# Optimization experiments

Hardware: AMD Instinct MI355X
Metric: run time of the kernel (lower is better)

The kernel has to match this reference:

```python
import jax, jax.numpy as jnp
import numpy as np

B, S_ENC, S_DEC, ENC_H, DEC_H = 8, 2048, 2048, 512, 512


def setup_inputs() -> dict:
    key = jax.random.key(0)
    k1, k2, k3 = jax.random.split(key, 3)
    return {
        "enc_hidden_states": jax.random.normal(k1, (B, S_ENC, ENC_H), dtype=jnp.float32),
        "dec_hidden_states": jax.random.normal(k2, (B, S_DEC, DEC_H), dtype=jnp.float32),
        "W_att": jax.random.normal(k3, (ENC_H, DEC_H), dtype=jnp.float32),
    }


def reference(enc_hidden_states, dec_hidden_states, W_att):
    # Project encoder states: [B, S_enc, dec_h]
    enc_proj = jnp.einsum("bse,ed->bsd", enc_hidden_states, W_att)
    # Luong 'general' scores for all decoder timesteps at once: [B, S_dec, S_enc]
    # (original code loops over decoder timesteps via tf.map_fn; this is the
    # equivalent single batched matmul)
    att_logits = jnp.einsum("btd,bsd->bts", dec_hidden_states, enc_proj)
    att_softmax = jax.nn.softmax(att_logits, axis=-1)
    # Attention context vectors: [B, S_dec, enc_h]
    att_vector = jnp.einsum("bts,bse->bte", att_softmax, enc_hidden_states)
    return att_vector
```

## Files before the change

kernel.cpp:

```cpp
#include <hip/hip_runtime.h>
#include <cstdint>


#define DEVINL __device__ __forceinline__

typedef __attribute__((ext_vector_type(8))) short short8;
typedef __attribute__((ext_vector_type(4))) float f32x4;

DEVINL short f2bf(float x) {
    union { float f; uint32_t u; } v; v.f = x;
    uint32_t r = v.u + 0x7FFFu + ((v.u >> 16) & 1u);
    return (short)(r >> 16);
}
DEVINL float bf2f(short h) {
    union { uint32_t u; float f; } v; v.u = ((uint32_t)(uint16_t)h) << 16;
    return v.f;
}

DEVINL void gload_lds16(const void* g, void* l) {
    __builtin_amdgcn_global_load_lds(
        (const __attribute__((address_space(1))) char*)g,
        (__attribute__((address_space(3))) char*)l, 16, 0, 0);
}

__global__ __launch_bounds__(256)
void split_kernel(const float* __restrict__ x, short* __restrict__ hi,
                  short* __restrict__ lo)
{
    long i = ((long)blockIdx.x * 256 + threadIdx.x) * 8;
    f32x4 a = *(const f32x4*)(x + i);
    f32x4 b = *(const f32x4*)(x + i + 4);
    short8 h, l;
#pragma unroll
    for (int j = 0; j < 4; j++) {
        short ha = f2bf(a[j]); h[j] = ha;     l[j] = f2bf(a[j] - bf2f(ha));
        short hb = f2bf(b[j]); h[4 + j] = hb; l[4 + j] = f2bf(b[j] - bf2f(hb));
    }
    *(short8*)(hi + i) = h;
    *(short8*)(lo + i) = l;
}

__global__ __launch_bounds__(256)
void split_w_kernel(const float* __restrict__ w, short* __restrict__ wth,
                    short* __restrict__ wtl)
{
    int idx = blockIdx.x * 256 + threadIdx.x;
    int k = idx >> 9, n = idx & 511;
    float v = w[idx];
    short h = f2bf(v);
    wth[(long)n * 512 + k] = h;
    wtl[(long)n * 512 + k] = f2bf(v - bf2f(h));
}

__global__ __launch_bounds__(256)
void split_transpose_kernel(const float* __restrict__ x, short* __restrict__ hi,
                            short* __restrict__ lo, short* __restrict__ xt)
{
    __shared__ short tile[32][33];
    const int b  = blockIdx.z;
    const int s0 = blockIdx.x * 32;
    const int e0 = blockIdx.y * 32;
    const float* px = x + (long)b * 2048 * 512;
    short* ph = hi + (long)b * 2048 * 512;
    short* pl = lo + (long)b * 2048 * 512;
    short* pt = xt + (long)b * 512 * 2048;
    const int tx = threadIdx.x & 31;
    const int ty = threadIdx.x >> 5;
#pragma unroll
    for (int r = 0; r < 32; r += 8) {
        long idx = (long)(s0 + ty + r) * 512 + e0 + tx;
        float v = px[idx];
        short h = f2bf(v);
        ph[idx] = h;
        pl[idx] = f2bf(v - bf2f(h));
        tile[ty + r][tx] = h;
    }
    __syncthreads();
#pragma unroll
    for (int r = 0; r < 32; r += 8)
        pt[(long)(e0 + ty + r) * 2048 + s0 + tx] = tile[tx][ty + r];
}

template<int NTERMS, bool SPLIT_OUT>
__global__ __launch_bounds__(256, 2)
void gemm_bt(const short* __restrict__ Ah, const short* __restrict__ Al,
             const short* __restrict__ Bh, const short* __restrict__ Bl,
             float* __restrict__ C, short* __restrict__ Ch, short* __restrict__ Cl,
             int K, int lda, int ldb, int ldc,
             long sA, long sB, long sC)
{
    extern __shared__ char smem_raw[];
    constexpr int OPS = (NTERMS == 3) ? 4 : 2;
    constexpr int SET = 128 * 32 * OPS;
    short* smem = (short*)smem_raw;

    const int tid  = threadIdx.x;
    const int wave = tid >> 6;
    const int lane = tid & 63;
    const int quad = lane >> 4;
    const int l16  = lane & 15;
    const int wm   = (wave >> 1) * 64;
    const int wn   = (wave & 1) * 64;

    const long tile_m = (long)blockIdx.y * 128;
    const long tile_n = (long)blockIdx.x * 128;
    const int  bz     = blockIdx.z;

    const short* pAh = Ah + (long)bz * sA;
    const short* pBh = Bh + (long)bz * sB;
    const short* pAl = (NTERMS == 3) ? (Al + (long)bz * sA) : nullptr;
    const short* pBl = (NTERMS == 3) ? (Bl + (long)bz * sB) : nullptr;

    const int srow = tid >> 2;
    const int skq  = (tid & 3) * 8;
    const int lds_off = srow * 32 + skq;
    const long ga0 = (tile_m + srow) * (long)lda + skq;
    const long gb0 = (tile_n + srow) * (long)ldb + skq;

    auto stage = [&](int k0, int buf) {
        short* s   = smem + buf * SET;
        short* ash = s;
        short* bsh = s + 128 * 32;
        gload_lds16(pAh + ga0 + k0,             ash + lds_off);
        gload_lds16(pAh + ga0 + 64l * lda + k0, ash + lds_off + 64 * 32);
        gload_lds16(pBh + gb0 + k0,             bsh + lds_off);
        gload_lds16(pBh + gb0 + 64l * ldb + k0, bsh + lds_off + 64 * 32);
        if constexpr (NTERMS == 3) {
            short* asl = s + 2 * 128 * 32;
            short* bsl = s + 3 * 128 * 32;
            gload_lds16(pAl + ga0 + k0,             asl + lds_off);
            gload_lds16(pAl + ga0 + 64l * lda + k0, asl + lds_off + 64 * 32);
            gload_lds16(pBl + gb0 + k0,             bsl + lds_off);
            gload_lds16(pBl + gb0 + 64l * ldb + k0, bsl + lds_off + 64 * 32);
        }
    };

    f32x4 acc[4][4] = {};
    stage(0, 0);
    int cur = 0;

    for (int k0 = 0; k0 < K; k0 += 32) {
        __syncthreads();
        if (k0 + 32 < K) stage(k0 + 32, cur ^ 1);

        short* s   = smem + cur * SET;
        short* ash = s;
        short* bsh = s + 128 * 32;
        short* asl = s + 2 * 128 * 32;
        short* bsl = s + 3 * 128 * 32;

        short8 ah[4], bh[4], al[4], bl[4];
#pragma unroll
        for (int i = 0; i < 4; i++) {
            ah[i] = *(const short8*)&ash[(wm + i * 16 + l16) * 32 + quad * 8];
            bh[i] = *(const short8*)&bsh[(wn + i * 16 + l16) * 32 + quad * 8];
            if constexpr (NTERMS == 3) {
                al[i] = *(const short8*)&asl[(wm + i * 16 + l16) * 32 + quad * 8];
                bl[i] = *(const short8*)&bsl[(wn + i * 16 + l16) * 32 + quad * 8];
            }
        }
#pragma unroll
        for (int i = 0; i < 4; i++)
#pragma unroll
            for (int j = 0; j < 4; j++) {
                acc[i][j] = __builtin_amdgcn_mfma_f32_16x16x32_bf16(ah[i], bh[j], acc[i][j], 0, 0, 0);
                if constexpr (NTERMS == 3) {
                    acc[i][j] = __builtin_amdgcn_mfma_f32_16x16x32_bf16(ah[i], bl[j], acc[i][j], 0, 0, 0);
                    acc[i][j] = __builtin_amdgcn_mfma_f32_16x16x32_bf16(al[i], bh[j], acc[i][j], 0, 0, 0);
                }
            }
        cur ^= 1;
    }

#pragma unroll
    for (int i = 0; i < 4; i++)
#pragma unroll
        for (int j = 0; j < 4; j++) {
            const long row0 = tile_m + wm + i * 16 + quad * 4;
            const long col  = tile_n + wn + j * 16 + l16;
#pragma unroll
            for (int r = 0; r < 4; r++) {
                float v = acc[i][j][r];
                if constexpr (SPLIT_OUT) {
                    long idx = (long)bz * sC + (row0 + r) * (long)ldc + col;
                    short h = f2bf(v);
                    Ch[idx] = h;
                    Cl[idx] = f2bf(v - bf2f(h));
                } else {
                    C[(long)bz * sC + (row0 + r) * (long)ldc + col] = v;
                }
            }
        }
}

__global__ __launch_bounds__(512, 2)
void gemm3_256(const short* __restrict__ Ah, const short* __restrict__ Al,
               const short* __restrict__ Bh, const short* __restrict__ Bl,
               short* __restrict__ Pt, float* __restrict__ stats,
               int K, int lda, int ldb,
               long sA, long sB, int nbx, int nby)
{
    extern __shared__ char smem_raw[];
    short* smem = (short*)smem_raw;
    constexpr int PL  = 256 * 32;
    constexpr int SET = 4 * PL;

    const int t    = threadIdx.x;
    const int wave = t >> 6;
    const int lane = t & 63;
    const int quad = lane >> 4;
    const int l16  = lane & 15;
    const int wm   = (wave >> 2) * 128;
    const int wn   = (wave & 3) * 64;
    const int kslot8 = ((quad ^ ((l16 >> 1) & 3)) << 3);

    const int nwg = gridDim.x;
    const int wg  = blockIdx.x;
    const int swz = (wg & 7) * (nwg >> 3) + (wg >> 3);
    const int per_b = nbx * nby;
    const int bz  = swz / per_b;
    const int rem = swz - bz * per_b;
    const long tile_m = (long)(rem / nbx) * 256;
    const long tile_n = (long)(rem % nbx) * 256;

    const short* pAh = Ah + (long)bz * sA;
    const short* pAl = Al + (long)bz * sA;
    const short* pBh = Bh + (long)bz * sB;
    const short* pBl = Bl + (long)bz * sB;

    const int srow   = t >> 2;
    const int schunk = (t & 3) ^ ((t >> 3) & 3);
    const long gA  = (tile_m + srow) * (long)lda + schunk * 8;
    const long gB  = (tile_n + srow) * (long)ldb + schunk * 8;
    const long gA2 = gA + 128l * lda;
    const long gB2 = gB + 128l * ldb;
    const int ld0 = t * 8;

    f32x4 acc[8][4] = {};

    {
        short* s = smem;
        gload_lds16(pAh + gA,  s + ld0);
        gload_lds16(pAh + gA2, s + ld0 + 4096);
        gload_lds16(pBh + gB,  s + 2 * PL + ld0);
        gload_lds16(pBh + gB2, s + 2 * PL + ld0 + 4096);
        gload_lds16(pAl + gA,  s + PL + ld0);
        gload_lds16(pAl + gA2, s + PL + ld0 + 4096);
        gload_lds16(pBl + gB,  s + 3 * PL + ld0);
        gload_lds16(pBl + gB2, s + 3 * PL + ld0 + 4096);
    }
    asm volatile("s_waitcnt vmcnt(4)" ::: "memory");
    __builtin_amdgcn_s_barrier();

    const int NT = K >> 5;
    int cur = 0;
#pragma unroll 1
    for (int kt = 0; kt < NT; ++kt) {
        const short* s    = smem + cur * SET;
        short* sn         = smem + (cur ^ 1) * SET;
        const short* ah_p = s;
        const short* al_p = s + PL;
        const short* bh_p = s + 2 * PL;
        const short* bl_p = s + 3 * PL;
        const int  k0n  = (kt + 1) << 5;
        const bool more = (kt + 1 < NT);

        short8 ahA[4], ahB[4], xbh[4], xbl[4], xal[4];

#pragma unroll
        for (int i = 0; i < 4; i++)
            ahA[i] = *(const short8*)&ah_p[(wm + i * 16 + l16) * 32 + kslot8];
#pragma unroll
        for (int j = 0; j < 4; j++)
            xbh[j] = *(const short8*)&bh_p[(wn + j * 16 + l16) * 32 + kslot8];
        if (more) {
            gload_lds16(pAh + gA  + k0n, sn + ld0);
            gload_lds16(pAh + gA2 + k0n, sn + ld0 + 4096);
        }
        __builtin_amdgcn_s_barrier();
        asm volatile("s_waitcnt lgkmcnt(0)" ::: "memory");
        __builtin_amdgcn_sched_barrier(0);
        __builtin_amdgcn_s_setprio(1);
#pragma unroll
        for (int i = 0; i < 4; i++)
#pragma unroll
            for (int j = 0; j < 4; j++)
                acc[i][j] = __builtin_amdgcn_mfma_f32_16x16x32_bf16(ahA[i], xbh[j], acc[i][j], 0, 0, 0);
        __builtin_amdgcn_s_setprio(0);

#pragma unroll
        for (int i = 0; i < 4; i++)
            ahB[i] = *(const short8*)&ah_p[(wm + 64 + i * 16 + l16) * 32 + kslot8];
        if (more) {
            gload_lds16(pBh + gB  + k0n, sn + 2 * PL + ld0);
            gload_lds16(pBh + gB2 + k0n, sn + 2 * PL + ld0 + 4096);
            asm volatile("s_waitcnt vmcnt(6)" ::: "memory");
        } else {
            asm volatile("s_waitcnt vmcnt(2)" ::: "memory");
        }
        __builtin_amdgcn_s_barrier();
        asm volatile("s_waitcnt lgkmcnt(0)" ::: "memory");
        __builtin_amdgcn_sched_barrier(0);
        __builtin_amdgcn_s_setprio(1);
#pragma unroll
        for (int i = 0; i < 4; i++)
#pragma unroll
            for (int j = 0; j < 4; j++)
                acc[4 + i][j] = __builtin_amdgcn_mfma_f32_16x16x32_bf16(ahB[i], xbh[j], acc[4 + i][j], 0, 0, 0);
        __builtin_amdgcn_s_setprio(0);

#pragma unroll
        for (int i = 0; i < 4; i++)
            xal[i] = *(const short8*)&al_p[(wm + i * 16 + l16) * 32 + kslot8];
        if (more) {
            gload_lds16(pAl + gA  + k0n, sn + PL + ld0);
            gload_lds16(pAl + gA2 + k0n, sn + PL + ld0 + 4096);
        }
        __builtin_amdgcn_s_barrier();
        asm volatile("s_waitcnt lgkmcnt(0)" ::: "memory");
        __builtin_amdgcn_sched_barrier(0);
        __builtin_amdgcn_s_setprio(1);
#pragma unroll
        for (int i = 0; i < 4; i++)
#pragma unroll
            for (int j = 0; j < 4; j++)
                acc[i][j] = __builtin_amdgcn_mfma_f32_16x16x32_bf16(xal[i], xbh[j], acc[i][j], 0, 0, 0);
        __builtin_amdgcn_s_setprio(0);

#pragma unroll
        for (int i = 0; i < 4; i++)
            xal[i] = *(const short8*)&al_p[(wm + 64 + i * 16 + l16) * 32 + kslot8];
        if (more) {
            gload_lds16(pBl + gB  + k0n, sn + 3 * PL + ld0);
            gload_lds16(pBl + gB2 + k0n, sn + 3 * PL + ld0 + 4096);
            asm volatile("s_waitcnt vmcnt(8)" ::: "memory");
        } else {
            asm volatile("s_waitcnt vmcnt(0)" ::: "memory");
        }
        __builtin_amdgcn_s_barrier();
        asm volatile("s_waitcnt lgkmcnt(0)" ::: "memory");
        __builtin_amdgcn_sched_barrier(0);
        __builtin_amdgcn_s_setprio(1);
#pragma unroll
        for (int i = 0; i < 4; i++)
#pragma unroll
            for (int j = 0; j < 4; j++)
                acc[4 + i][j] = __builtin_amdgcn_mfma_f32_16x16x32_bf16(xal[i], xbh[j], acc[4 + i][j], 0, 0, 0);
        __builtin_amdgcn_s_setprio(0);

#pragma unroll
        for (int j = 0; j < 4; j++)
            xbl[j] = *(const short8*)&bl_p[(wn + j * 16 + l16) * 32 + kslot8];
        __builtin_amdgcn_s_barrier();
        asm volatile("s_waitcnt lgkmcnt(0)" ::: "memory");
        __builtin_amdgcn_sched_barrier(0);
        __builtin_amdgcn_s_setprio(1);
#pragma unroll
        for (int i = 0; i < 4; i++)
#pragma unroll
            for (int j = 0; j < 4; j++)
                acc[i][j] = __builtin_amdgcn_mfma_f32_16x16x32_bf16(ahA[i], xbl[j], acc[i][j], 0, 0, 0);
        __builtin_amdgcn_s_setprio(0);

        __builtin_amdgcn_s_setprio(1);
#pragma unroll
        for (int i = 0; i < 4; i++)
#pragma unroll
            for (int j = 0; j < 4; j++)
                acc[4 + i][j] = __builtin_amdgcn_mfma_f32_16x16x32_bf16(ahB[i], xbl[j], acc[4 + i][j], 0, 0, 0);
        __builtin_amdgcn_s_setprio(0);
        if (more) {
            asm volatile("s_waitcnt vmcnt(4)" ::: "memory");
            __builtin_amdgcn_s_barrier();
        }

        cur ^= 1;
    }

    float* sf   = (float*)smem_raw;
    float* lmax = sf;
    float* rowm = sf + 1024;
    const int wr = wave >> 2, wc = wave & 3;
    __syncthreads();

#pragma unroll
    for (int i = 0; i < 8; i++)
#pragma unroll
        for (int r = 0; r < 4; r++) {
            float m = acc[i][0][r];
#pragma unroll
            for (int j = 1; j < 4; j++) m = fmaxf(m, acc[i][j][r]);
#pragma unroll
            for (int o = 1; o < 16; o <<= 1) m = fmaxf(m, __shfl_xor(m, o));
            if (l16 == 0) lmax[wc * 256 + wr * 128 + i * 16 + quad * 4 + r] = m;
        }
    __syncthreads();
    if (t < 256)
        rowm[t] = fmaxf(fmaxf(lmax[t], lmax[256 + t]),
                        fmaxf(lmax[512 + t], lmax[768 + t]));
    __syncthreads();
    float* lsum = sf;
    short* PtB  = Pt + (long)bz * 2048 * 2048;
#pragma unroll
    for (int i = 0; i < 8; i++)
#pragma unroll
        for (int r = 0; r < 4; r++) {
            const int rit = wr * 128 + i * 16 + quad * 4 + r;
            const float m = rowm[rit];
            float sum = 0.f;
#pragma unroll
            for (int j = 0; j < 4; j++) {
                float e = __expf(acc[i][j][r] - m);
                sum += e;
                PtB[(tile_m + rit) * 2048 + tile_n + wn + j * 16 + l16] = f2bf(e);
            }
#pragma unroll
            for (int o = 1; o < 16; o <<= 1) sum += __shfl_xor(sum, o);
            if (l16 == 0) lsum[wc * 256 + rit] = sum;
        }
    __syncthreads();
    if (t < 256) {
        float S = lsum[t] + lsum[256 + t] + lsum[512 + t] + lsum[768 + t];
        const long sidx = (((long)bz * 2048 + tile_m + t) * 8 + (tile_n >> 8)) * 2;
        stats[sidx]     = rowm[t];
        stats[sidx + 1] = S;
    }
}

__global__ __launch_bounds__(256)
void combine_kernel(const float* __restrict__ stats, float* __restrict__ scales)
{
    const long row = (long)blockIdx.x * 256 + threadIdx.x;
    const float* p = stats + row * 16;
    float m[8], s[8];
#pragma unroll
    for (int t = 0; t < 8; t++) { m[t] = p[t * 2]; s[t] = p[t * 2 + 1]; }
    float M = m[0];
#pragma unroll
    for (int t = 1; t < 8; t++) M = fmaxf(M, m[t]);
    float S = 0.f;
#pragma unroll
    for (int t = 0; t < 8; t++) S += s[t] * __expf(m[t] - M);
    const float inv = 1.f / S;
#pragma unroll
    for (int t = 0; t < 8; t++)
        scales[row * 8 + t] = __expf(m[t] - M) * inv;
}

__global__ __launch_bounds__(256, 2)
void gemm_pv(const short* __restrict__ A, const short* __restrict__ B,
             const float* __restrict__ scales, float* __restrict__ C,
             int K, int lda, int ldb, int ldc,
             long sA, long sB, long sC)
{
    extern __shared__ char smem_raw[];
    constexpr int SET = 128 * 32 * 2;
    short* smem = (short*)smem_raw;

    const int tid  = threadIdx.x;
    const int wave = tid >> 6;
    const int lane = tid & 63;
    const int quad = lane >> 4;
    const int l16  = lane & 15;
    const int wm   = (wave >> 1) * 64;
    const int wn   = (wave & 1) * 64;

    const long tile_m = (long)blockIdx.y * 128;
    const long tile_n = (long)blockIdx.x * 128;
    const int  bz     = blockIdx.z;

    const short* pA = A + (long)bz * sA;
    const short* pB = B + (long)bz * sB;

    const int srow = tid >> 2;
    const int skq  = (tid & 3) * 8;
    const int lds_off = srow * 32 + skq;
    const long ga0 = (tile_m + srow) * (long)lda + skq;
    const long gb0 = (tile_n + srow) * (long)ldb + skq;

    auto stage = [&](int k0, int buf) {
        short* s   = smem + buf * SET;
        short* ash = s;
        short* bsh = s + 128 * 32;
        gload_lds16(pA + ga0 + k0,             ash + lds_off);
        gload_lds16(pA + ga0 + 64l * lda + k0, ash + lds_off + 64 * 32);
        gload_lds16(pB + gb0 + k0,             bsh + lds_off);
        gload_lds16(pB + gb0 + 64l * ldb + k0, bsh + lds_off + 64 * 32);
    };

    f32x4 acc[4][4] = {};
    f32x4 oacc[4][4] = {};
    const f32x4 vzero = {0.f, 0.f, 0.f, 0.f};
    stage(0, 0);
    int cur = 0;

    for (int k0 = 0; k0 < K; k0 += 32) {
        __syncthreads();
        if (k0 + 32 < K) stage(k0 + 32, cur ^ 1);

        short* s   = smem + cur * SET;
        short* ash = s;
        short* bsh = s + 128 * 32;

        short8 ah[4], bh[4];
#pragma unroll
        for (int i = 0; i < 4; i++) {
            ah[i] = *(const short8*)&ash[(wm + i * 16 + l16) * 32 + quad * 8];
            bh[i] = *(const short8*)&bsh[(wn + i * 16 + l16) * 32 + quad * 8];
        }
#pragma unroll
        for (int i = 0; i < 4; i++)
#pragma unroll
            for (int j = 0; j < 4; j++)
                acc[i][j] = __builtin_amdgcn_mfma_f32_16x16x32_bf16(ah[i], bh[j], acc[i][j], 0, 0, 0);

        if (((k0 + 32) & 255) == 0) {
            const int tt = k0 >> 8;
#pragma unroll
            for (int i = 0; i < 4; i++) {
                f32x4 sv;
#pragma unroll
                for (int r = 0; r < 4; r++)
                    sv[r] = scales[((long)bz * 2048 + tile_m + wm + i * 16 + quad * 4 + r) * 8 + tt];
#pragma unroll
                for (int j = 0; j < 4; j++) {
                    oacc[i][j] += sv * acc[i][j];
                    acc[i][j] = vzero;
                }
            }
        }
        cur ^= 1;
    }

#pragma unroll
    for (int i = 0; i < 4; i++)
#pragma unroll
        for (int j = 0; j < 4; j++) {
            const long row0 = tile_m + wm + i * 16 + quad * 4;
            const long col  = tile_n + wn + j * 16 + l16;
#pragma unroll
            for (int r = 0; r < 4; r++)
                C[(long)bz * sC + (row0 + r) * (long)ldc + col] = oacc[i][j][r];
        }
}

extern "C" void kernel_launch(void* const* d_in, const int* in_sizes, int n_in,
                              void* d_out, int out_size, void* d_ws, size_t ws_size,
                              hipStream_t stream)
{
    const float* enc = (const float*)d_in[0];
    const float* dec = (const float*)d_in[1];
    const float* W   = (const float*)d_in[2];
    float* out = (float*)d_out;

    const long BSE = 8l * 2048 * 512;
    const long NW  = 512l * 512;

    char* p = (char*)d_ws;
    auto take = [&](long bytes) { char* r = p; p += (bytes + 255) & ~255l; return r; };
    short* enc_hi = (short*)take(BSE * 2);
    short* enc_lo = (short*)take(BSE * 2);
    short* dec_hi = (short*)take(BSE * 2);
    short* dec_lo = (short*)take(BSE * 2);
    short* ep_hi  = (short*)take(BSE * 2);
    short* ep_lo  = (short*)take(BSE * 2);
    short* enc_t  = (short*)take(BSE * 2);
    short* wt_hi  = (short*)take(NW * 2);
    short* wt_lo  = (short*)take(NW * 2);
    short* Pt     = (short*)take(8l * 2048 * 2048 * 2);
    float* stats  = (float*)take(8l * 2048 * 8 * 2 * 4);
    float* scales = (float*)take(8l * 2048 * 8 * 4);
    (void)ws_size; (void)in_sizes; (void)n_in; (void)out_size;

    static bool attr_set = false;
    if (!attr_set) {
        (void)hipFuncSetAttribute((const void*)gemm3_256,
                                  hipFuncAttributeMaxDynamicSharedMemorySize,
                                  131072);
        attr_set = true;
    }

    split_transpose_kernel<<<dim3(64, 16, 8), 256, 0, stream>>>(
        enc, enc_hi, enc_lo, enc_t);
    split_kernel<<<4096, 256, 0, stream>>>(dec, dec_hi, dec_lo);
    split_w_kernel<<<1024, 256, 0, stream>>>(W, wt_hi, wt_lo);

    gemm_bt<3, true><<<dim3(4, 128, 1), 256, 64 * 1024, stream>>>(
        enc_hi, enc_lo, wt_hi, wt_lo, nullptr, ep_hi, ep_lo,
        512, 512, 512, 512, 0, 0, 0);

    gemm3_256<<<512, 512, 131072, stream>>>(
        dec_hi, dec_lo, ep_hi, ep_lo, Pt, stats,
        512, 512, 512, 2048l * 512, 2048l * 512, 8, 8);

    combine_kernel<<<64, 256, 0, stream>>>(stats, scales);

    gemm_pv<<<dim3(4, 16, 8), 256, 32 * 1024, stream>>>(
        Pt, enc_t, scales, out,
        2048, 2048, 2048, 512, 2048l * 2048, 512l * 2048, 2048l * 512);
}
```

Measured before the change: 319.5 us.

## Fuse decoder fp32-to-bf16 hi/lo split into the score GEMM A-tile loader

Drops the separate split kernel for decoder states. The score GEMM now reads fp32 decoder rows directly into registers, splits them into bf16 hi/lo inside the kernel and writes both to LDS. This removes one launch and a full round trip of bf16 hi/lo decoder data through global memory. In exchange the GEMM reads twice the A bytes as fp32, spends extra VALU on the conversion, and reorders its vmcnt waits in the pipeline, which adds register pressure and latency risk.

```diff
diff --git a/kernel.cpp b/kernel.cpp
--- a/kernel.cpp
+++ b/kernel.cpp
@@ -21,23 +21,6 @@
     __builtin_amdgcn_global_load_lds(
         (const __attribute__((address_space(1))) char*)g,
         (__attribute__((address_space(3))) char*)l, 16, 0, 0);
-}
-
-__global__ __launch_bounds__(256)
-void split_kernel(const float* __restrict__ x, short* __restrict__ hi,
-                  short* __restrict__ lo)
-{
-    long i = ((long)blockIdx.x * 256 + threadIdx.x) * 8;
-    f32x4 a = *(const f32x4*)(x + i);
-    f32x4 b = *(const f32x4*)(x + i + 4);
-    short8 h, l;
-#pragma unroll
-    for (int j = 0; j < 4; j++) {
-        short ha = f2bf(a[j]); h[j] = ha;     l[j] = f2bf(a[j] - bf2f(ha));
-        short hb = f2bf(b[j]); h[4 + j] = hb; l[4 + j] = f2bf(b[j] - bf2f(hb));
-    }
-    *(short8*)(hi + i) = h;
-    *(short8*)(lo + i) = l;
 }
 
 __global__ __launch_bounds__(256)
@@ -194,11 +177,9 @@
 }
 
 __global__ __launch_bounds__(512, 2)
-void gemm3_256(const short* __restrict__ Ah, const short* __restrict__ Al,
-               const short* __restrict__ Bh, const short* __restrict__ Bl,
-               short* __restrict__ Pt, float* __restrict__ stats,
-               int K, int lda, int ldb,
-               long sA, long sB, int nbx, int nby)
+void gemm3_256(const float* __restrict__ Dec, const short* __restrict__ Bh,
+               const short* __restrict__ Bl, short* __restrict__ Pt,
+               float* __restrict__ stats, int nbx, int nby)
 {
     extern __shared__ char smem_raw[];
     short* smem = (short*)smem_raw;
@@ -223,39 +204,68 @@
     const long tile_m = (long)(rem / nbx) * 256;
     const long tile_n = (long)(rem % nbx) * 256;
 
-    const short* pAh = Ah + (long)bz * sA;
-    const short* pAl = Al + (long)bz * sA;
-    const short* pBh = Bh + (long)bz * sB;
-    const short* pBl = Bl + (long)bz * sB;
+    const float* pDec = Dec + (long)bz * 2048 * 512;
+    const short* pBh  = Bh + (long)bz * 2048 * 512;
+    const short* pBl  = Bl + (long)bz * 2048 * 512;
 
     const int srow   = t >> 2;
     const int schunk = (t & 3) ^ ((t >> 3) & 3);
-    const long gA  = (tile_m + srow) * (long)lda + schunk * 8;
-    const long gB  = (tile_n + srow) * (long)ldb + schunk * 8;
-    const long gA2 = gA + 128l * lda;
-    const long gB2 = gB + 128l * ldb;
+    const long gB  = (tile_n + srow) * 512l + schunk * 8;
+    const long gB2 = gB + 128l * 512;
     const int ld0 = t * 8;
 
+    const int srowA = t >> 1;
+    const int kA0   = (t & 1) * 16;
+    const long gAf  = (tile_m + srowA) * 512l + kA0;
+    const int xrA   = (srowA >> 1) & 3;
+    const int c0    = kA0 >> 3;
+    const int wA0   = srowA * 32 + ((c0 ^ xrA) << 3);
+    const int wA1   = srowA * 32 + (((c0 + 1) ^ xrA) << 3);
+
+    f32x4 af[4];
+    auto loadA = [&](int k0) {
+#pragma unroll
+        for (int q = 0; q < 4; q++)
+            af[q] = *(const f32x4*)(pDec + gAf + k0 + q * 4);
+    };
+    auto writeA = [&](int buf) {
+        short8 h0, h1, l0, l1;
+#pragma unroll
+        for (int e = 0; e < 8; e++) {
+            float v = af[e >> 2][e & 3];
+            short hh = f2bf(v);
+            h0[e] = hh; l0[e] = f2bf(v - bf2f(hh));
+        }
+#pragma unroll
+        for (int e = 0; e < 8; e++) {
+            float v = af[2 + (e >> 2)][e & 3];
+            short hh = f2bf(v);
+            h1[e] = hh; l1[e] = f2bf(v - bf2f(hh));
+        }
+        short* sp = smem + buf * SET;
+        *(short8*)&sp[wA0]      = h0;
+        *(short8*)&sp[wA1]      = h1;
+        *(short8*)&sp[PL + wA0] = l0;
+        *(short8*)&sp[PL + wA1] = l1;
+    };
+
     f32x4 acc[8][4] = {};
 
-    {
-        short* s = smem;
-        gload_lds16(pAh + gA,  s + ld0);
-        gload_lds16(pAh + gA2, s + ld0 + 4096);
-        gload_lds16(pBh + gB,  s + 2 * PL + ld0);
-        gload_lds16(pBh + gB2, s + 2 * PL + ld0 + 4096);
-        gload_lds16(pAl + gA,  s + PL + ld0);
-        gload_lds16(pAl + gA2, s + PL + ld0 + 4096);
-        gload_lds16(pBl + gB,  s + 3 * PL + ld0);
-        gload_lds16(pBl + gB2, s + 3 * PL + ld0 + 4096);
-    }
-    asm volatile("s_waitcnt vmcnt(4)" ::: "memory");
+    loadA(0);
+    __builtin_amdgcn_sched_barrier(0);
+    gload_lds16(pBh + gB,  smem + 2 * PL + ld0);
+    gload_lds16(pBh + gB2, smem + 2 * PL + ld0 + 4096);
+    gload_lds16(pBl + gB,  smem + 3 * PL + ld0);
+    gload_lds16(pBl + gB2, smem + 3 * PL + ld0 + 4096);
+    __builtin_amdgcn_sched_barrier(0);
+    asm volatile("s_waitcnt vmcnt(2)" ::: "memory");
+    writeA(0);
+    asm volatile("s_waitcnt lgkmcnt(0)" ::: "memory");
     __builtin_amdgcn_s_barrier();
 
-    const int NT = K >> 5;
     int cur = 0;
 #pragma unroll 1
-    for (int kt = 0; kt < NT; ++kt) {
+    for (int kt = 0; kt < 16; ++kt) {
         const short* s    = smem + cur * SET;
         short* sn         = smem + (cur ^ 1) * SET;
         const short* ah_p = s;
@@ -263,7 +273,7 @@
         const short* bh_p = s + 2 * PL;
         const short* bl_p = s + 3 * PL;
         const int  k0n  = (kt + 1) << 5;
-        const bool more = (kt + 1 < NT);
+        const bool more = (kt + 1 < 16);
 
         short8 ahA[4], ahB[4], xbh[4], xbl[4], xal[4];
 
@@ -273,10 +283,6 @@
 #pragma unroll
         for (int j = 0; j < 4; j++)
             xbh[j] = *(const short8*)&bh_p[(wn + j * 16 + l16) * 32 + kslot8];
-        if (more) {
-            gload_lds16(pAh + gA  + k0n, sn + ld0);
-            gload_lds16(pAh + gA2 + k0n, sn + ld0 + 4096);
-        }
         __builtin_amdgcn_s_barrier();
         asm volatile("s_waitcnt lgkmcnt(0)" ::: "memory");
         __builtin_amdgcn_sched_barrier(0);
@@ -294,9 +300,6 @@
         if (more) {
             gload_lds16(pBh + gB  + k0n, sn + 2 * PL + ld0);
             gload_lds16(pBh + gB2 + k0n, sn + 2 * PL + ld0 + 4096);
-            asm volatile("s_waitcnt vmcnt(6)" ::: "memory");
-        } else {
-            asm volatile("s_waitcnt vmcnt(2)" ::: "memory");
         }
         __builtin_amdgcn_s_barrier();
         asm volatile("s_waitcnt lgkmcnt(0)" ::: "memory");
@@ -313,8 +316,10 @@
         for (int i = 0; i < 4; i++)
             xal[i] = *(const short8*)&al_p[(wm + i * 16 + l16) * 32 + kslot8];
         if (more) {
-            gload_lds16(pAl + gA  + k0n, sn + PL + ld0);
-            gload_lds16(pAl + gA2 + k0n, sn + PL + ld0 + 4096);
+            loadA(k0n);
+            __builtin_amdgcn_sched_barrier(0);
+            gload_lds16(pBl + gB  + k0n, sn + 3 * PL + ld0);
+            gload_lds16(pBl + gB2 + k0n, sn + 3 * PL + ld0 + 4096);
         }
         __builtin_amdgcn_s_barrier();
         asm volatile("s_waitcnt lgkmcnt(0)" ::: "memory");
@@ -330,13 +335,10 @@
 #pragma unroll
         for (int i = 0; i < 4; i++)
             xal[i] = *(const short8*)&al_p[(wm + 64 + i * 16 + l16) * 32 + kslot8];
-        if (more) {
-            gload_lds16(pBl + gB  + k0n, sn + 3 * PL + ld0);
-            gload_lds16(pBl + gB2 + k0n, sn + 3 * PL + ld0 + 4096);
+        if (more)
             asm volatile("s_waitcnt vmcnt(8)" ::: "memory");
-        } else {
+        else
             asm volatile("s_waitcnt vmcnt(0)" ::: "memory");
-        }
         __builtin_amdgcn_s_barrier();
         asm volatile("s_waitcnt lgkmcnt(0)" ::: "memory");
         __builtin_amdgcn_sched_barrier(0);
@@ -351,6 +353,10 @@
 #pragma unroll
         for (int j = 0; j < 4; j++)
             xbl[j] = *(const short8*)&bl_p[(wn + j * 16 + l16) * 32 + kslot8];
+        if (more) {
+            asm volatile("s_waitcnt vmcnt(2)" ::: "memory");
+            writeA(cur ^ 1);
+        }
         __builtin_amdgcn_s_barrier();
         asm volatile("s_waitcnt lgkmcnt(0)" ::: "memory");
         __builtin_amdgcn_sched_barrier(0);
@@ -369,10 +375,8 @@
             for (int j = 0; j < 4; j++)
                 acc[4 + i][j] = __builtin_amdgcn_mfma_f32_16x16x32_bf16(ahB[i], xbl[j], acc[4 + i][j], 0, 0, 0);
         __builtin_amdgcn_s_setprio(0);
-        if (more) {
-            asm volatile("s_waitcnt vmcnt(4)" ::: "memory");
+        if (more)
             __builtin_amdgcn_s_barrier();
-        }
 
         cur ^= 1;
     }
@@ -560,8 +564,6 @@
     auto take = [&](long bytes) { char* r = p; p += (bytes + 255) & ~255l; return r; };
     short* enc_hi = (short*)take(BSE * 2);
     short* enc_lo = (short*)take(BSE * 2);
-    short* dec_hi = (short*)take(BSE * 2);
-    short* dec_lo = (short*)take(BSE * 2);
     short* ep_hi  = (short*)take(BSE * 2);
     short* ep_lo  = (short*)take(BSE * 2);
     short* enc_t  = (short*)take(BSE * 2);
@@ -582,7 +584,6 @@
 
     split_transpose_kernel<<<dim3(64, 16, 8), 256, 0, stream>>>(
         enc, enc_hi, enc_lo, enc_t);
-    split_kernel<<<4096, 256, 0, stream>>>(dec, dec_hi, dec_lo);
     split_w_kernel<<<1024, 256, 0, stream>>>(W, wt_hi, wt_lo);
 
     gemm_bt<3, true><<<dim3(4, 128, 1), 256, 64 * 1024, stream>>>(
@@ -590,8 +591,7 @@
         512, 512, 512, 512, 0, 0, 0);
 
     gemm3_256<<<512, 512, 131072, stream>>>(
-        dec_hi, dec_lo, ep_hi, ep_lo, Pt, stats,
-        512, 512, 512, 2048l * 512, 2048l * 512, 8, 8);
+        dec, ep_hi, ep_lo, Pt, stats, 8, 8);
 
     combine_kernel<<<64, 256, 0, stream>>>(stats, scales);
 
```

Result: slower. 372.0 us (+16.4%).
